# Kernel tuning notes

Measured on AMD Instinct MI355X. Metric: run time of the kernel, lower is better.

The kernel has to match this reference:

```python
import jax, jax.numpy as jnp
import numpy as np

# Fixed tetrahedral (kanchor=4) rotation->anchor permutation table, taken verbatim
# from the docstring in the original source (trace_idx_ori).
TRACE_IDX_ORI = jnp.array([
    [0, 1, 2, 3], [0, 2, 3, 1], [0, 3, 1, 2],
    [1, 2, 0, 3], [1, 0, 3, 2], [1, 3, 2, 0],
    [2, 3, 0, 1], [2, 0, 1, 3], [2, 1, 3, 0],
    [3, 1, 0, 2], [3, 0, 2, 1], [3, 2, 1, 0]], dtype=jnp.int32)

B, A, N, M, D, H = 1, 4, 384, 384, 256, 8
C = D // H  # d_model_per_head = 32
NR = TRACE_IDX_ORI.shape[0]  # 12 rotations


def _project_heads(x, W, b):
    # x: (b, a, n, d) -> (b, a, h, n, c)
    y = x @ W.T + b
    bb, aa, nn, _ = y.shape
    return y.reshape(bb, aa, nn, H, C).transpose(0, 1, 3, 2, 4)


def setup_inputs() -> dict:
    key = jax.random.key(0)
    ks = jax.random.split(key, 6)
    s = 1.0 / np.sqrt(D).astype(np.float32)
    return {
        "input_q": jax.random.normal(ks[0], (B, A, N, D), dtype=jnp.float32),
        "input_k": jax.random.normal(ks[1], (B, A, M, D), dtype=jnp.float32),
        "input_v": jax.random.normal(ks[2], (B, A, M, D), dtype=jnp.float32),
        "Wq": jax.random.normal(ks[3], (D, D), dtype=jnp.float32) * s,
        "bq": jnp.zeros((D,), dtype=jnp.float32),
        "Wk": jax.random.normal(ks[4], (D, D), dtype=jnp.float32) * s,
        "bk": jnp.zeros((D,), dtype=jnp.float32),
        "Wv": jax.random.normal(ks[5], (D, D), dtype=jnp.float32) * s,
        "bv": jnp.zeros((D,), dtype=jnp.float32),
    }


def reference(input_q, input_k, input_v, Wq, bq, Wk, bk, Wv, bv):
    # Step 0: linear projections + split heads.  q,k,v: (b, a, h, n|m, c)
    q = _project_heads(input_q, Wq, bq)
    k = _project_heads(input_k, Wk, bk)
    v = _project_heads(input_v, Wv, bv)

    # Step 1: per-anchor-pair local attention scores: (b, a, e, h, n, m)
    scores_ae = jnp.einsum('bahnc,behmc->baehnm', q, k) / jnp.sqrt(
        jnp.asarray(C, dtype=q.dtype))

    # Step 2: rotation-wise gather (attn_mode='r_soft', alternative_impl=False).
    # For rotation r, query anchor a attends to key anchor trace_idx_ori[r, a]:
    # scores_rot[b, r, a] = scores_ae[b, a, trace_idx_ori[r, a]]  -> (b, nr, a, h, n, m)
    a_idx = jnp.arange(A, dtype=jnp.int32)[None, :]  # (1, A) broadcasts vs (NR, A)
    scores_rot = scores_ae[:, a_idx, TRACE_IDX_ORI]

    # Global rotation attention: pool over anchors/heads/points (attn_r_summ='mean',
    # attn_r_multihead=False), make non-negative ('sq'), normalize over rotations.
    pooled = jnp.mean(scores_rot, axis=(2, 3, 4, 5))  # (b, nr)
    pos = pooled * pooled
    attn_r = pos / jnp.sum(pos, axis=-1, keepdims=True)  # (b, nr)

    # Step 3+4: softmax over key points per rotation, gather values per rotation,
    # then weight by the global rotation attention.
    attn_local = jax.nn.softmax(scores_rot, axis=-1)  # (b, nr, a, h, n, m)
    v_rot = v[:, TRACE_IDX_ORI]  # (b, nr, a, h, m, c)
    hidden = jnp.einsum('br,brahnm,brahmc->bahnc', attn_r, attn_local, v_rot)

    # Merge heads: (b, a, h, n, c) -> (b, a, n, h*c)
    out = hidden.transpose(0, 1, 3, 2, 4).reshape(B, A, N, D)
    return out
```

## Files before the change

kernel.cpp:

```cpp
#include <hip/hip_runtime.h>
#include <hip/hip_bf16.h>

typedef __attribute__((ext_vector_type(8))) short s8x8;
typedef __attribute__((ext_vector_type(4))) float f32x4;

union FragU { s8x8 v; unsigned d[4]; };

__device__ __forceinline__ ushort f2bf(float x) {
    union { float f; unsigned u; } c; c.f = x;
    unsigned r = c.u + 0x7FFFu + ((c.u >> 16) & 1u);
    return (ushort)(r >> 16);
}
__device__ __forceinline__ float bf2f(ushort b) {
    union { unsigned u; float f; } c; c.u = ((unsigned)b) << 16;
    return c.f;
}
__device__ __forceinline__ unsigned cvt_pk(float lo, float hi) {
    unsigned r;
    asm("v_cvt_pk_bf16_f32 %0, %1, %2" : "=v"(r) : "v"(lo), "v"(hi));
    return r;
}
__device__ __forceinline__ float asf(unsigned u) {
    union { unsigned u; float f; } c; c.u = u; return c.f;
}

__global__ __launch_bounds__(256) void proj_kernel(
    const float* __restrict__ Xq, const float* __restrict__ Xk,
    const float* __restrict__ Xv,
    const float* __restrict__ Wq, const float* __restrict__ bq,
    const float* __restrict__ Wk, const float* __restrict__ bk,
    const float* __restrict__ Wv, const float* __restrict__ bv,
    ushort* __restrict__ qh, ushort* __restrict__ ql,
    ushort* __restrict__ kh, ushort* __restrict__ kl,
    ushort* __restrict__ vh, float* __restrict__ part)
{
    __shared__ float csum[4][64];

    const int z = blockIdx.z;
    const float* X    = (z == 0) ? Xq : (z == 1) ? Xk : Xv;
    const float* W    = (z == 0) ? Wq : (z == 1) ? Wk : Wv;
    const float* bias = (z == 0) ? bq : (z == 1) ? bk : bv;

    const int tid  = threadIdx.x;
    const int wave = tid >> 6;
    const int lane = tid & 63;
    const int lg   = lane >> 4;
    const int ll   = lane & 15;
    const int row0 = blockIdx.x * 128 + wave * 32;
    const int col0 = blockIdx.y * 64;

    f32x4 acc[2][4];
    #pragma unroll
    for (int rt = 0; rt < 2; ++rt)
        #pragma unroll
        for (int ct = 0; ct < 4; ++ct) acc[rt][ct] = (f32x4){0.f, 0.f, 0.f, 0.f};

    for (int kk = 0; kk < 8; ++kk) {
        FragU ah[2], al[2];
        #pragma unroll
        for (int rt = 0; rt < 2; ++rt) {
            const float* xp = &X[(size_t)(row0 + rt * 16 + ll) * 256 + kk * 32 + lg * 8];
            const float4 x0 = *(const float4*)&xp[0];
            const float4 x1 = *(const float4*)&xp[4];
            const float xv[8] = {x0.x, x0.y, x0.z, x0.w, x1.x, x1.y, x1.z, x1.w};
            #pragma unroll
            for (int i = 0; i < 4; ++i) {
                const unsigned hd = cvt_pk(xv[2 * i], xv[2 * i + 1]);
                ah[rt].d[i] = hd;
                al[rt].d[i] = cvt_pk(xv[2 * i]     - asf(hd << 16),
                                     xv[2 * i + 1] - asf(hd & 0xffff0000u));
            }
        }
        #pragma unroll
        for (int ct = 0; ct < 4; ++ct) {
            const float* wp = &W[(size_t)(col0 + ct * 16 + ll) * 256 + kk * 32 + lg * 8];
            const float4 w0 = *(const float4*)&wp[0];
            const float4 w1 = *(const float4*)&wp[4];
            const float wv[8] = {w0.x, w0.y, w0.z, w0.w, w1.x, w1.y, w1.z, w1.w};
            FragU bh, bl;
            #pragma unroll
            for (int i = 0; i < 4; ++i) {
                const unsigned hd = cvt_pk(wv[2 * i], wv[2 * i + 1]);
                bh.d[i] = hd;
                bl.d[i] = cvt_pk(wv[2 * i]     - asf(hd << 16),
                                 wv[2 * i + 1] - asf(hd & 0xffff0000u));
            }
            #pragma unroll
            for (int rt = 0; rt < 2; ++rt) {
                acc[rt][ct] = __builtin_amdgcn_mfma_f32_16x16x32_bf16(ah[rt].v, bh.v, acc[rt][ct], 0, 0, 0);
                acc[rt][ct] = __builtin_amdgcn_mfma_f32_16x16x32_bf16(al[rt].v, bh.v, acc[rt][ct], 0, 0, 0);
                acc[rt][ct] = __builtin_amdgcn_mfma_f32_16x16x32_bf16(ah[rt].v, bl.v, acc[rt][ct], 0, 0, 0);
            }
        }
    }

    const int bx = blockIdx.x;
    const int ae = bx / 3;
    float bct[4];
    #pragma unroll
    for (int ct = 0; ct < 4; ++ct) bct[ct] = bias[col0 + ct * 16 + ll];

    if (z != 2) {
        #pragma unroll
        for (int rt = 0; rt < 2; ++rt) {
            #pragma unroll
            for (int ct = 0; ct < 4; ++ct) {
                const int d = col0 + ct * 16 + ll;
                const int hd = d >> 5;
                const int c = d & 31;
                #pragma unroll
                for (int j = 0; j < 4; ++j) {
                    const int n = (bx - ae * 3) * 128 + wave * 32 + rt * 16 + lg * 4 + j;
                    const float v = acc[rt][ct][j] + bct[ct];
                    const ushort hb = f2bf(v);
                    const ushort lb = f2bf(v - bf2f(hb));
                    if (z == 0) {
                        const size_t idx = ((size_t)((ae * 8 + hd) * 384 + n)) * 32 + c;
                        qh[idx] = hb; ql[idx] = lb;
                    } else {
                        const size_t idx =
                            ((size_t)(((ae * 8 + hd) * 4 + (c >> 3)) * 384 + n)) * 8 + (c & 7);
                        kh[idx] = hb; kl[idx] = lb;
                    }
                }
            }
        }
        #pragma unroll
        for (int ct = 0; ct < 4; ++ct) {
            float cs = 8.f * bct[ct];
            #pragma unroll
            for (int rt = 0; rt < 2; ++rt)
                #pragma unroll
                for (int j = 0; j < 4; ++j) cs += acc[rt][ct][j];
            cs += __shfl_xor(cs, 16);
            cs += __shfl_xor(cs, 32);
            if (lg == 0) csum[wave][ct * 16 + ll] = cs;
        }
        __syncthreads();
        if (tid < 64) {
            const float s = csum[0][tid] + csum[1][tid] + csum[2][tid] + csum[3][tid];
            part[((size_t)(z * 4 + ae) * 3 + (bx - ae * 3)) * 256 + blockIdx.y * 64 + tid] = s;
        }
    } else {
        #pragma unroll
        for (int rt = 0; rt < 2; ++rt) {
            #pragma unroll
            for (int ct = 0; ct < 4; ++ct) {
                const int d = col0 + ct * 16 + ll;
                const int hd = d >> 5;
                const int c = d & 31;
                ushort p[4];
                #pragma unroll
                for (int j = 0; j < 4; ++j) p[j] = f2bf(acc[rt][ct][j] + bct[ct]);
                const int m0 = (bx - ae * 3) * 128 + wave * 32 + rt * 16 + lg * 4;
                const size_t basei = ((size_t)((ae * 8 + hd) * 32 + c)) * 384 + m0;
                *(uint2*)&vh[basei] =
                    make_uint2((unsigned)p[0] | ((unsigned)p[1] << 16),
                               (unsigned)p[2] | ((unsigned)p[3] << 16));
            }
        }
    }
}

__global__ __launch_bounds__(192) void attn_mfma_kernel(
    const ushort* __restrict__ qhb, const ushort* __restrict__ qlb,
    const ushort* __restrict__ khb, const ushort* __restrict__ klb,
    const ushort* __restrict__ vhb, float* __restrict__ Sout)
{
    __shared__ ushort Kh[4 * 1544];
    __shared__ ushort Kl[4 * 1544];
    __shared__ ushort Vh[32 * 200];
    __shared__ ushort Pl[3 * 2 * 16 * 40];

    const int strip = blockIdx.x;
    const int aeh   = blockIdx.y;
    const int hh    = aeh & 7;
    const int ee    = (aeh >> 3) & 3;
    const int aa    = aeh >> 5;
    const int e8h   = ee * 8 + hh;
    const int a8h   = aa * 8 + hh;
    const int tid   = threadIdx.x;
    const int wave  = tid >> 6;
    const int lane  = tid & 63;
    const int lg    = lane >> 4;
    const int ll    = lane & 15;

    s8x8 qfh[2], qfl[2];
    #pragma unroll
    for (int r = 0; r < 2; ++r) {
        const int n0 = strip * 96 + (2 * wave + r) * 16;
        const size_t off = (size_t)(a8h * 384 + n0 + ll) * 32 + lg * 8;
        qfh[r] = *(const s8x8*)&qhb[off];
        qfl[r] = *(const s8x8*)&qlb[off];
    }

    f32x4 oacc[2][2];
    #pragma unroll
    for (int r = 0; r < 2; ++r)
        #pragma unroll
        for (int ct = 0; ct < 2; ++ct)
            oacc[r][ct] = (f32x4){0.f, 0.f, 0.f, 0.f};
    float lsum[2][4];
    #pragma unroll
    for (int r = 0; r < 2; ++r)
        #pragma unroll
        for (int j = 0; j < 4; ++j) lsum[r][j] = 0.f;
    const float sc = 0.17677669529663687f;

    for (int half = 0; half < 2; ++half) {
        #pragma unroll
        for (int i = 0; i < 4; ++i) {
            const size_t src = ((size_t)(e8h * 4 + i) * 384 + half * 192 + tid) * 8;
            *(uint4*)&Kh[i * 1544 + tid * 8] = *(const uint4*)&khb[src];
            *(uint4*)&Kl[i * 1544 + tid * 8] = *(const uint4*)&klb[src];
        }
        #pragma unroll
        for (int i = 0; i < 4; ++i) {
            const int u = tid + 192 * i;
            const int c = u / 24;
            const int m8 = (u - c * 24) * 8;
            *(uint4*)&Vh[c * 200 + m8] =
                *(const uint4*)&vhb[(size_t)(e8h * 32 + c) * 384 + half * 192 + m8];
        }
        __syncthreads();

        for (int mt2 = 0; mt2 < 6; ++mt2) {
            #pragma unroll
            for (int sub = 0; sub < 2; ++sub) {
                const int mt = mt2 * 2 + sub;
                const s8x8 kfh = *(const s8x8*)&Kh[lg * 1544 + (mt * 16 + ll) * 8];
                const s8x8 kfl = *(const s8x8*)&Kl[lg * 1544 + (mt * 16 + ll) * 8];
                #pragma unroll
                for (int r = 0; r < 2; ++r) {
                    f32x4 s = {0.f, 0.f, 0.f, 0.f};
                    __builtin_amdgcn_s_setprio(1);
                    s = __builtin_amdgcn_mfma_f32_16x16x32_bf16(qfh[r], kfh, s, 0, 0, 0);
                    s = __builtin_amdgcn_mfma_f32_16x16x32_bf16(qfl[r], kfh, s, 0, 0, 0);
                    s = __builtin_amdgcn_mfma_f32_16x16x32_bf16(qfh[r], kfl, s, 0, 0, 0);
                    __builtin_amdgcn_s_setprio(0);
                    #pragma unroll
                    for (int j = 0; j < 4; ++j) {
                        const float p = __expf(s[j] * sc);
                        lsum[r][j] += p;
                        Pl[((wave * 2 + r) * 16 + lg * 4 + j) * 40 + sub * 16 + ll] = f2bf(p);
                    }
                }
            }
            const int mloc = mt2 * 32;
            const s8x8 vf0 = *(const s8x8*)&Vh[(0  + ll) * 200 + mloc + lg * 8];
            const s8x8 vf1 = *(const s8x8*)&Vh[(16 + ll) * 200 + mloc + lg * 8];
            #pragma unroll
            for (int r = 0; r < 2; ++r) {
                const s8x8 pa = *(const s8x8*)&Pl[((wave * 2 + r) * 16 + ll) * 40 + lg * 8];
                __builtin_amdgcn_s_setprio(1);
                oacc[r][0] = __builtin_amdgcn_mfma_f32_16x16x32_bf16(pa, vf0, oacc[r][0], 0, 0, 0);
                oacc[r][1] = __builtin_amdgcn_mfma_f32_16x16x32_bf16(pa, vf1, oacc[r][1], 0, 0, 0);
                __builtin_amdgcn_s_setprio(0);
            }
        }
        __syncthreads();
    }

    #pragma unroll
    for (int r = 0; r < 2; ++r) {
        #pragma unroll
        for (int j = 0; j < 4; ++j) {
            float L = lsum[r][j];
            L += __shfl_xor(L, 1);
            L += __shfl_xor(L, 2);
            L += __shfl_xor(L, 4);
            L += __shfl_xor(L, 8);
            const float invL = 1.f / L;
            const int row = strip * 96 + (2 * wave + r) * 16 + lg * 4 + j;
            const size_t base = (size_t)(aeh * 384 + row) * 32;
            Sout[base + 0  + ll] = oacc[r][0][j] * invL;
            Sout[base + 16 + ll] = oacc[r][1][j] * invL;
        }
    }
}

__global__ __launch_bounds__(256) void combine_kernel(
    const float* __restrict__ S, const float* __restrict__ part,
    float* __restrict__ out)
{
    __shared__ float ws4[4][16];
    __shared__ float cellsh[16];
    __shared__ float wsh[16];
    const int tid = threadIdx.x;
    const int lane = tid & 63;
    const int wv = tid >> 6;

    float qs[4], ks[4];
    #pragma unroll
    for (int a2 = 0; a2 < 4; ++a2) {
        const float* pq = &part[(size_t)(0 * 4 + a2) * 3 * 256 + tid];
        const float* pk = &part[(size_t)(1 * 4 + a2) * 3 * 256 + tid];
        qs[a2] = pq[0] + pq[256] + pq[512];
        ks[a2] = pk[0] + pk[256] + pk[512];
    }
    #pragma unroll
    for (int i = 0; i < 16; ++i) {
        float v = qs[i >> 2] * ks[i & 3];
        v += __shfl_xor(v, 1);
        v += __shfl_xor(v, 2);
        v += __shfl_xor(v, 4);
        v += __shfl_xor(v, 8);
        v += __shfl_xor(v, 16);
        v += __shfl_xor(v, 32);
        if (lane == 0) ws4[wv][i] = v;
    }
    __syncthreads();
    if (tid < 16)
        cellsh[tid] = 0.17677669529663687f *
            (ws4[0][tid] + ws4[1][tid] + ws4[2][tid] + ws4[3][tid]);
    __syncthreads();
    if (tid == 0) {
        const int TR[12][4] = {
            {0,1,2,3},{0,2,3,1},{0,3,1,2},{1,2,0,3},{1,0,3,2},{1,3,2,0},
            {2,3,0,1},{2,0,1,3},{2,1,3,0},{3,1,0,2},{3,0,2,1},{3,2,1,0}};
        const float denom = 4.0f * 8.0f * 384.0f * 384.0f;
        float pos[12];
        float psum = 0.f;
        for (int r = 0; r < 12; ++r) {
            float s = 0.f;
            for (int a2 = 0; a2 < 4; ++a2) s += cellsh[a2 * 4 + TR[r][a2]];
            const float pooled = s / denom;
            pos[r] = pooled * pooled;
            psum += pos[r];
        }
        float w[16];
        for (int i = 0; i < 16; ++i) w[i] = 0.f;
        const float ip = 1.f / psum;
        for (int r = 0; r < 12; ++r)
            for (int a2 = 0; a2 < 4; ++a2) w[a2 * 4 + TR[r][a2]] += pos[r] * ip;
        for (int i = 0; i < 16; ++i) wsh[i] = w[i];
    }
    __syncthreads();

    const int idx4 = blockIdx.x * 256 + tid;
    const int a = idx4 / 24576;
    const int rem = idx4 - a * 24576;
    const int n = rem >> 6;
    const int d4 = rem & 63;
    const int h = d4 >> 3;
    const int c0 = (d4 & 7) * 4;
    float4 r = make_float4(0.f, 0.f, 0.f, 0.f);
    #pragma unroll
    for (int e = 0; e < 4; ++e) {
        const float wv2 = wsh[a * 4 + e];
        const float4 s = *(const float4*)&S[(size_t)(((a * 4 + e) * 8 + h) * 384 + n) * 32 + c0];
        r.x += wv2 * s.x; r.y += wv2 * s.y; r.z += wv2 * s.z; r.w += wv2 * s.w;
    }
    *(float4*)&out[(size_t)idx4 * 4] = r;
}

extern "C" void kernel_launch(void* const* d_in, const int* in_sizes, int n_in,
                              void* d_out, int out_size, void* d_ws, size_t ws_size,
                              hipStream_t stream)
{
    const float* in_q = (const float*)d_in[0];
    const float* in_k = (const float*)d_in[1];
    const float* in_v = (const float*)d_in[2];
    const float* Wq   = (const float*)d_in[3];
    const float* bq   = (const float*)d_in[4];
    const float* Wk   = (const float*)d_in[5];
    const float* bk   = (const float*)d_in[6];
    const float* Wv   = (const float*)d_in[7];
    const float* bv   = (const float*)d_in[8];

    ushort* qh = (ushort*)d_ws;
    ushort* ql = qh + 393216;
    ushort* kh = ql + 393216;
    ushort* kl = kh + 393216;
    ushort* vh = kl + 393216;
    float*  Sb = (float*)(vh + 393216);
    float*  pt = Sb + 1572864;
    float*  outp = (float*)d_out;

    dim3 pgrid(12, 4, 3);
    proj_kernel<<<pgrid, 256, 0, stream>>>(in_q, in_k, in_v, Wq, bq, Wk, bk,
                                           Wv, bv, qh, ql, kh, kl, vh, pt);
    dim3 agrid(4, 128);
    attn_mfma_kernel<<<agrid, 192, 0, stream>>>(qh, ql, kh, kl, vh, Sb);
    combine_kernel<<<384, 256, 0, stream>>>(Sb, pt, outp);
}
```

Before: 47.23 us.

## Split projection into many single-wave blocks and move rotation stats to own kernel

The projection kernel goes from 144 blocks of four waves (128 rows each) to 1152 single-wave blocks (16 rows each), so more CUs get work in this small GEMM. Column sums now go straight to a larger partial buffer with no shared-memory reduction. The rotation-weight computation moves out of every combine block into a separate one-block stats kernel, so combine blocks no longer repeat it. This adds an extra launch and less weight-fragment reuse per block, meaning more redundant global loads and bf16 split conversions of W.

```diff
diff --git a/kernel.cpp b/kernel.cpp
--- a/kernel.cpp
+++ b/kernel.cpp
@@ -24,7 +24,7 @@
     union { unsigned u; float f; } c; c.u = u; return c.f;
 }
 
-__global__ __launch_bounds__(256) void proj_kernel(
+__global__ __launch_bounds__(64) void proj_kernel(
     const float* __restrict__ Xq, const float* __restrict__ Xk,
     const float* __restrict__ Xv,
     const float* __restrict__ Wq, const float* __restrict__ bq,
@@ -34,41 +34,35 @@
     ushort* __restrict__ kh, ushort* __restrict__ kl,
     ushort* __restrict__ vh, float* __restrict__ part)
 {
-    __shared__ float csum[4][64];
-
     const int z = blockIdx.z;
     const float* X    = (z == 0) ? Xq : (z == 1) ? Xk : Xv;
     const float* W    = (z == 0) ? Wq : (z == 1) ? Wk : Wv;
     const float* bias = (z == 0) ? bq : (z == 1) ? bk : bv;
 
-    const int tid  = threadIdx.x;
-    const int wave = tid >> 6;
-    const int lane = tid & 63;
+    const int lane = threadIdx.x;
     const int lg   = lane >> 4;
     const int ll   = lane & 15;
-    const int row0 = blockIdx.x * 128 + wave * 32;
+    const int bx   = blockIdx.x;
+    const int row0 = bx * 16;
     const int col0 = blockIdx.y * 64;
 
-    f32x4 acc[2][4];
-    #pragma unroll
-    for (int rt = 0; rt < 2; ++rt)
-        #pragma unroll
-        for (int ct = 0; ct < 4; ++ct) acc[rt][ct] = (f32x4){0.f, 0.f, 0.f, 0.f};
+    f32x4 acc[4];
+    #pragma unroll
+    for (int ct = 0; ct < 4; ++ct) acc[ct] = (f32x4){0.f, 0.f, 0.f, 0.f};
 
     for (int kk = 0; kk < 8; ++kk) {
-        FragU ah[2], al[2];
-        #pragma unroll
-        for (int rt = 0; rt < 2; ++rt) {
-            const float* xp = &X[(size_t)(row0 + rt * 16 + ll) * 256 + kk * 32 + lg * 8];
+        FragU ah, al;
+        {
+            const float* xp = &X[(size_t)(row0 + ll) * 256 + kk * 32 + lg * 8];
             const float4 x0 = *(const float4*)&xp[0];
             const float4 x1 = *(const float4*)&xp[4];
             const float xv[8] = {x0.x, x0.y, x0.z, x0.w, x1.x, x1.y, x1.z, x1.w};
             #pragma unroll
             for (int i = 0; i < 4; ++i) {
                 const unsigned hd = cvt_pk(xv[2 * i], xv[2 * i + 1]);
-                ah[rt].d[i] = hd;
-                al[rt].d[i] = cvt_pk(xv[2 * i]     - asf(hd << 16),
-                                     xv[2 * i + 1] - asf(hd & 0xffff0000u));
+                ah.d[i] = hd;
+                al.d[i] = cvt_pk(xv[2 * i]     - asf(hd << 16),
+                                 xv[2 * i + 1] - asf(hd & 0xffff0000u));
             }
         }
         #pragma unroll
@@ -85,80 +79,126 @@
                 bl.d[i] = cvt_pk(wv[2 * i]     - asf(hd << 16),
                                  wv[2 * i + 1] - asf(hd & 0xffff0000u));
             }
-            #pragma unroll
-            for (int rt = 0; rt < 2; ++rt) {
-                acc[rt][ct] = __builtin_amdgcn_mfma_f32_16x16x32_bf16(ah[rt].v, bh.v, acc[rt][ct], 0, 0, 0);
-                acc[rt][ct] = __builtin_amdgcn_mfma_f32_16x16x32_bf16(al[rt].v, bh.v, acc[rt][ct], 0, 0, 0);
-                acc[rt][ct] = __builtin_amdgcn_mfma_f32_16x16x32_bf16(ah[rt].v, bl.v, acc[rt][ct], 0, 0, 0);
-            }
-        }
-    }
-
-    const int bx = blockIdx.x;
-    const int ae = bx / 3;
+            acc[ct] = __builtin_amdgcn_mfma_f32_16x16x32_bf16(ah.v, bh.v, acc[ct], 0, 0, 0);
+            acc[ct] = __builtin_amdgcn_mfma_f32_16x16x32_bf16(al.v, bh.v, acc[ct], 0, 0, 0);
+            acc[ct] = __builtin_amdgcn_mfma_f32_16x16x32_bf16(ah.v, bl.v, acc[ct], 0, 0, 0);
+        }
+    }
+
+    const int ae  = bx / 24;
+    const int rbl = bx - ae * 24;
     float bct[4];
     #pragma unroll
     for (int ct = 0; ct < 4; ++ct) bct[ct] = bias[col0 + ct * 16 + ll];
 
     if (z != 2) {
         #pragma unroll
-        for (int rt = 0; rt < 2; ++rt) {
-            #pragma unroll
-            for (int ct = 0; ct < 4; ++ct) {
-                const int d = col0 + ct * 16 + ll;
-                const int hd = d >> 5;
-                const int c = d & 31;
-                #pragma unroll
-                for (int j = 0; j < 4; ++j) {
-                    const int n = (bx - ae * 3) * 128 + wave * 32 + rt * 16 + lg * 4 + j;
-                    const float v = acc[rt][ct][j] + bct[ct];
-                    const ushort hb = f2bf(v);
-                    const ushort lb = f2bf(v - bf2f(hb));
-                    if (z == 0) {
-                        const size_t idx = ((size_t)((ae * 8 + hd) * 384 + n)) * 32 + c;
-                        qh[idx] = hb; ql[idx] = lb;
-                    } else {
-                        const size_t idx =
-                            ((size_t)(((ae * 8 + hd) * 4 + (c >> 3)) * 384 + n)) * 8 + (c & 7);
-                        kh[idx] = hb; kl[idx] = lb;
-                    }
+        for (int ct = 0; ct < 4; ++ct) {
+            const int d = col0 + ct * 16 + ll;
+            const int hd = d >> 5;
+            const int c = d & 31;
+            #pragma unroll
+            for (int j = 0; j < 4; ++j) {
+                const int n = rbl * 16 + lg * 4 + j;
+                const float v = acc[ct][j] + bct[ct];
+                const ushort hb = f2bf(v);
+                const ushort lb = f2bf(v - bf2f(hb));
+                if (z == 0) {
+                    const size_t idx = ((size_t)((ae * 8 + hd) * 384 + n)) * 32 + c;
+                    qh[idx] = hb; ql[idx] = lb;
+                } else {
+                    const size_t idx =
+                        ((size_t)(((ae * 8 + hd) * 4 + (c >> 3)) * 384 + n)) * 8 + (c & 7);
+                    kh[idx] = hb; kl[idx] = lb;
                 }
             }
         }
         #pragma unroll
         for (int ct = 0; ct < 4; ++ct) {
-            float cs = 8.f * bct[ct];
-            #pragma unroll
-            for (int rt = 0; rt < 2; ++rt)
-                #pragma unroll
-                for (int j = 0; j < 4; ++j) cs += acc[rt][ct][j];
+            float cs = 4.f * bct[ct];
+            #pragma unroll
+            for (int j = 0; j < 4; ++j) cs += acc[ct][j];
             cs += __shfl_xor(cs, 16);
             cs += __shfl_xor(cs, 32);
-            if (lg == 0) csum[wave][ct * 16 + ll] = cs;
-        }
-        __syncthreads();
-        if (tid < 64) {
-            const float s = csum[0][tid] + csum[1][tid] + csum[2][tid] + csum[3][tid];
-            part[((size_t)(z * 4 + ae) * 3 + (bx - ae * 3)) * 256 + blockIdx.y * 64 + tid] = s;
+            if (lg == 0)
+                part[((size_t)(z * 4 + ae) * 24 + rbl) * 256 + col0 + ct * 16 + ll] = cs;
         }
     } else {
         #pragma unroll
-        for (int rt = 0; rt < 2; ++rt) {
-            #pragma unroll
-            for (int ct = 0; ct < 4; ++ct) {
-                const int d = col0 + ct * 16 + ll;
-                const int hd = d >> 5;
-                const int c = d & 31;
-                ushort p[4];
-                #pragma unroll
-                for (int j = 0; j < 4; ++j) p[j] = f2bf(acc[rt][ct][j] + bct[ct]);
-                const int m0 = (bx - ae * 3) * 128 + wave * 32 + rt * 16 + lg * 4;
-                const size_t basei = ((size_t)((ae * 8 + hd) * 32 + c)) * 384 + m0;
-                *(uint2*)&vh[basei] =
-                    make_uint2((unsigned)p[0] | ((unsigned)p[1] << 16),
-                               (unsigned)p[2] | ((unsigned)p[3] << 16));
-            }
-        }
+        for (int ct = 0; ct < 4; ++ct) {
+            const int d = col0 + ct * 16 + ll;
+            const int hd = d >> 5;
+            const int c = d & 31;
+            ushort p[4];
+            #pragma unroll
+            for (int j = 0; j < 4; ++j) p[j] = f2bf(acc[ct][j] + bct[ct]);
+            const int m0 = rbl * 16 + lg * 4;
+            const size_t basei = ((size_t)((ae * 8 + hd) * 32 + c)) * 384 + m0;
+            *(uint2*)&vh[basei] =
+                make_uint2((unsigned)p[0] | ((unsigned)p[1] << 16),
+                           (unsigned)p[2] | ((unsigned)p[3] << 16));
+        }
+    }
+}
+
+__global__ __launch_bounds__(256) void stats_kernel(
+    const float* __restrict__ part, float* __restrict__ wout)
+{
+    __shared__ float ws4[4][16];
+    __shared__ float cellsh[16];
+    const int tid = threadIdx.x;
+    const int lane = tid & 63;
+    const int wv = tid >> 6;
+
+    float qs[4], ks[4];
+    #pragma unroll
+    for (int a2 = 0; a2 < 4; ++a2) {
+        const float* pq = &part[(size_t)(0 * 4 + a2) * 24 * 256 + tid];
+        const float* pk = &part[(size_t)(1 * 4 + a2) * 24 * 256 + tid];
+        float sq = 0.f, sk = 0.f;
+        #pragma unroll
+        for (int r = 0; r < 24; ++r) {
+            sq += pq[r * 256];
+            sk += pk[r * 256];
+        }
+        qs[a2] = sq; ks[a2] = sk;
+    }
+    #pragma unroll
+    for (int i = 0; i < 16; ++i) {
+        float v = qs[i >> 2] * ks[i & 3];
+        v += __shfl_xor(v, 1);
+        v += __shfl_xor(v, 2);
+        v += __shfl_xor(v, 4);
+        v += __shfl_xor(v, 8);
+        v += __shfl_xor(v, 16);
+        v += __shfl_xor(v, 32);
+        if (lane == 0) ws4[wv][i] = v;
+    }
+    __syncthreads();
+    if (tid < 16)
+        cellsh[tid] = 0.17677669529663687f *
+            (ws4[0][tid] + ws4[1][tid] + ws4[2][tid] + ws4[3][tid]);
+    __syncthreads();
+    if (tid == 0) {
+        const int TR[12][4] = {
+            {0,1,2,3},{0,2,3,1},{0,3,1,2},{1,2,0,3},{1,0,3,2},{1,3,2,0},
+            {2,3,0,1},{2,0,1,3},{2,1,3,0},{3,1,0,2},{3,0,2,1},{3,2,1,0}};
+        const float denom = 4.0f * 8.0f * 384.0f * 384.0f;
+        float pos[12];
+        float psum = 0.f;
+        for (int r = 0; r < 12; ++r) {
+            float s = 0.f;
+            for (int a2 = 0; a2 < 4; ++a2) s += cellsh[a2 * 4 + TR[r][a2]];
+            const float pooled = s / denom;
+            pos[r] = pooled * pooled;
+            psum += pos[r];
+        }
+        float w[16];
+        for (int i = 0; i < 16; ++i) w[i] = 0.f;
+        const float ip = 1.f / psum;
+        for (int r = 0; r < 12; ++r)
+            for (int a2 = 0; a2 < 4; ++a2) w[a2 * 4 + TR[r][a2]] += pos[r] * ip;
+        for (int i = 0; i < 16; ++i) wout[i] = w[i];
     }
 }
 
@@ -280,61 +320,12 @@
 }
 
 __global__ __launch_bounds__(256) void combine_kernel(
-    const float* __restrict__ S, const float* __restrict__ part,
+    const float* __restrict__ S, const float* __restrict__ wbuf,
     float* __restrict__ out)
 {
-    __shared__ float ws4[4][16];
-    __shared__ float cellsh[16];
     __shared__ float wsh[16];
     const int tid = threadIdx.x;
-    const int lane = tid & 63;
-    const int wv = tid >> 6;
-
-    float qs[4], ks[4];
-    #pragma unroll
-    for (int a2 = 0; a2 < 4; ++a2) {
-        const float* pq = &part[(size_t)(0 * 4 + a2) * 3 * 256 + tid];
-        const float* pk = &part[(size_t)(1 * 4 + a2) * 3 * 256 + tid];
-        qs[a2] = pq[0] + pq[256] + pq[512];
-        ks[a2] = pk[0] + pk[256] + pk[512];
-    }
-    #pragma unroll
-    for (int i = 0; i < 16; ++i) {
-        float v = qs[i >> 2] * ks[i & 3];
-        v += __shfl_xor(v, 1);
-        v += __shfl_xor(v, 2);
-        v += __shfl_xor(v, 4);
-        v += __shfl_xor(v, 8);
-        v += __shfl_xor(v, 16);
-        v += __shfl_xor(v, 32);
-        if (lane == 0) ws4[wv][i] = v;
-    }
-    __syncthreads();
-    if (tid < 16)
-        cellsh[tid] = 0.17677669529663687f *
-            (ws4[0][tid] + ws4[1][tid] + ws4[2][tid] + ws4[3][tid]);
-    __syncthreads();
-    if (tid == 0) {
-        const int TR[12][4] = {
-            {0,1,2,3},{0,2,3,1},{0,3,1,2},{1,2,0,3},{1,0,3,2},{1,3,2,0},
-            {2,3,0,1},{2,0,1,3},{2,1,3,0},{3,1,0,2},{3,0,2,1},{3,2,1,0}};
-        const float denom = 4.0f * 8.0f * 384.0f * 384.0f;
-        float pos[12];
-        float psum = 0.f;
-        for (int r = 0; r < 12; ++r) {
-            float s = 0.f;
-            for (int a2 = 0; a2 < 4; ++a2) s += cellsh[a2 * 4 + TR[r][a2]];
-            const float pooled = s / denom;
-            pos[r] = pooled * pooled;
-            psum += pos[r];
-        }
-        float w[16];
-        for (int i = 0; i < 16; ++i) w[i] = 0.f;
-        const float ip = 1.f / psum;
-        for (int r = 0; r < 12; ++r)
-            for (int a2 = 0; a2 < 4; ++a2) w[a2 * 4 + TR[r][a2]] += pos[r] * ip;
-        for (int i = 0; i < 16; ++i) wsh[i] = w[i];
-    }
+    if (tid < 16) wsh[tid] = wbuf[tid];
     __syncthreads();
 
     const int idx4 = blockIdx.x * 256 + tid;
@@ -375,12 +366,14 @@
     ushort* vh = kl + 393216;
     float*  Sb = (float*)(vh + 393216);
     float*  pt = Sb + 1572864;
+    float*  wb = pt + 49152;
     float*  outp = (float*)d_out;
 
-    dim3 pgrid(12, 4, 3);
-    proj_kernel<<<pgrid, 256, 0, stream>>>(in_q, in_k, in_v, Wq, bq, Wk, bk,
-                                           Wv, bv, qh, ql, kh, kl, vh, pt);
+    dim3 pgrid(96, 4, 3);
+    proj_kernel<<<pgrid, 64, 0, stream>>>(in_q, in_k, in_v, Wq, bq, Wk, bk,
+                                          Wv, bv, qh, ql, kh, kl, vh, pt);
+    stats_kernel<<<1, 256, 0, stream>>>(pt, wb);
     dim3 agrid(4, 128);
     attn_mfma_kernel<<<agrid, 192, 0, stream>>>(qh, ql, kh, kl, vh, Sb);
-    combine_kernel<<<384, 256, 0, stream>>>(Sb, pt, outp);
-}
+    combine_kernel<<<384, 256, 0, stream>>>(Sb, wb, outp);
+}
```

After: 47.31 us. About the same (+0.2%).
